# Kernel tuning notes

Measured on AMD Instinct MI355X. Metric: run time of the kernel, lower is better.

The kernel has to match this reference:

```python
import jax, jax.numpy as jnp
import numpy as np

N_USER, N_TX, E = 50000, 50000, 600000
D_USER, D_TX, D_ALIGN, HID, OUT = 128, 64, 128, 256, 128


def setup_inputs() -> dict:
    key = jax.random.key(0)
    ks = jax.random.split(key, 16)
    s = 0.05
    return {
        "x_user": jax.random.normal(ks[0], (N_USER, D_USER), jnp.float32),
        "x_tx": jax.random.normal(ks[1], (N_TX, D_TX), jnp.float32),
        "edge_user_tx": jax.random.randint(ks[2], (2, E), 0, N_USER),
        "edge_tx_user": jax.random.randint(ks[3], (2, E), 0, N_TX),
        "W_align_user": jax.random.normal(ks[4], (D_USER, D_ALIGN), jnp.float32) * s,
        "b_align_user": jnp.zeros((D_ALIGN,), jnp.float32),
        "W_align_tx": jax.random.normal(ks[5], (D_TX, D_ALIGN), jnp.float32) * s,
        "b_align_tx": jnp.zeros((D_ALIGN,), jnp.float32),
        "eps_ut": jnp.zeros((), jnp.float32),
        "eps_tu": jnp.zeros((), jnp.float32),
        "W1_ut": jax.random.normal(ks[6], (D_TX + D_ALIGN, HID), jnp.float32) * s,
        "b1_ut": jnp.zeros((HID,), jnp.float32),
        "W2_ut": jax.random.normal(ks[7], (HID, OUT), jnp.float32) * s,
        "b2_ut": jnp.zeros((OUT,), jnp.float32),
        "W1_tu": jax.random.normal(ks[8], (D_USER + D_ALIGN, HID), jnp.float32) * s,
        "b1_tu": jnp.zeros((HID,), jnp.float32),
        "W2_tu": jax.random.normal(ks[9], (HID, OUT), jnp.float32) * s,
        "b2_tu": jnp.zeros((OUT,), jnp.float32),
    }


def _mlp(h, W1, b1, W2, b2):
    return jnp.maximum(h @ W1 + b1, 0.0) @ W2 + b2


def _hexgin_conv(x_src, x_dst, edge_index, W_a, b_a, eps, W1, b1, W2, b2):
    # align src features, gather along edges, scatter-sum into dst nodes
    a_src = x_src @ W_a + b_a                       # [N_src, D_ALIGN]
    msgs = a_src[edge_index[0]]                     # [E, D_ALIGN] gather
    agg = jax.ops.segment_sum(msgs, edge_index[1], num_segments=x_dst.shape[0])
    h = jnp.concatenate([(1.0 + eps) * x_dst, agg], axis=1)
    return _mlp(h, W1, b1, W2, b2)


def reference(x_user, x_tx, edge_user_tx, edge_tx_user,
              W_align_user, b_align_user, W_align_tx, b_align_tx,
              eps_ut, eps_tu,
              W1_ut, b1_ut, W2_ut, b2_ut,
              W1_tu, b1_tu, W2_tu, b2_tu):
    # relation (user, makes, tx): updates tx nodes
    out_tx = _hexgin_conv(x_user, x_tx, edge_user_tx,
                          W_align_user, b_align_user, eps_ut,
                          W1_ut, b1_ut, W2_ut, b2_ut)
    # relation (tx, to, user): updates user nodes
    out_user = _hexgin_conv(x_tx, x_user, edge_tx_user,
                            W_align_tx, b_align_tx, eps_tu,
                            W1_tu, b1_tu, W2_tu, b2_tu)
    # HeteroConv aggr='sum': single relation per target, so plain outputs
    return out_user, out_tx
```

## Files before the change

kernel.cpp:

```cpp
#include <hip/hip_runtime.h>
#include <hip/hip_bf16.h>


#define D_USER 128
#define D_TX 64
#define D_ALIGN 128
#define HID 256
#define OUT_D 128
#define NNODE 50000
#define SLOTS 64

typedef __attribute__((ext_vector_type(8))) short short8;
typedef __attribute__((ext_vector_type(4))) float f32x4;
typedef unsigned short ush;

struct alignas(8) us4 { ush x, y, z, w; };

__device__ __forceinline__ ush f2bf(float f) {
    union { float f; unsigned u; } v; v.f = f;
    unsigned u = v.u + 0x7fffu + ((v.u >> 16) & 1u);
    return (ush)(u >> 16);
}
__device__ __forceinline__ float2 bfu2f(unsigned u) {
    union { unsigned u; float f; } a, b;
    a.u = (u & 0xffffu) << 16;
    b.u = u & 0xffff0000u;
    return make_float2(a.f, b.f);
}
__device__ __forceinline__ unsigned f2bfu(float2 v) {
    return (unsigned)f2bf(v.x) | ((unsigned)f2bf(v.y) << 16);
}

__global__ void to_bf16_all(const float* __restrict__ xu, ush* __restrict__ xbu,
                            const float* __restrict__ xt, ush* __restrict__ xbt,
                            int n8u, int n8t)
{
    int i = blockIdx.x * blockDim.x + threadIdx.x;
    const float* x; ush* xb; int j;
    if (i < n8u) { x = xu; xb = xbu; j = i; }
    else if (i < n8u + n8t) { x = xt; xb = xbt; j = i - n8u; }
    else return;
    const float4 a = *reinterpret_cast<const float4*>(&x[(size_t)j * 8]);
    const float4 b = *reinterpret_cast<const float4*>(&x[(size_t)j * 8 + 4]);
    ush o[8];
    o[0] = f2bf(a.x); o[1] = f2bf(a.y); o[2] = f2bf(a.z); o[3] = f2bf(a.w);
    o[4] = f2bf(b.x); o[5] = f2bf(b.y); o[6] = f2bf(b.z); o[7] = f2bf(b.w);
    *reinterpret_cast<uint4*>(&xb[(size_t)j * 8]) = *reinterpret_cast<uint4*>(o);
}

__global__ void wprep(const float* __restrict__ Wa_u, const float* __restrict__ ba_u,
                      const float* __restrict__ W1_ut,
                      const float* __restrict__ Wa_t, const float* __restrict__ ba_t,
                      const float* __restrict__ W1_tu,
                      const float* __restrict__ W2_ut, const float* __restrict__ W2_tu,
                      ush* __restrict__ Bt1a, float* __restrict__ bfv1,
                      ush* __restrict__ Bt1b, float* __restrict__ bfv2,
                      ush* __restrict__ Bt2a, ush* __restrict__ Bt2b)
{
    const int KT = 192;
    const int SEG1 = HID * (KT + 1);
    const int SEG2 = OUT_D * HID;
    int idx = blockIdx.x * blockDim.x + threadIdx.x;
    if (idx < 2 * SEG1) {
        bool r2 = idx >= SEG1;
        int id = r2 ? idx - SEG1 : idx;
        const float* Wa = r2 ? Wa_t : Wa_u;
        const float* ba = r2 ? ba_t : ba_u;
        const float* W1 = r2 ? W1_tu : W1_ut;
        ush* Bt = r2 ? Bt1b : Bt1a;
        float* bfv = r2 ? bfv2 : bfv1;
        const int Dd = r2 ? 128 : 64;
        int c = id & (HID - 1);
        int k = id >> 8;
        const float* w1bot = W1 + (size_t)Dd * HID;
        if (k < Dd) {
            Bt[(size_t)c * KT + k] = f2bf(W1[(size_t)k * HID + c]);
        } else if (k < KT) {
            int ks = k - Dd;
            float acc = 0.f;
            for (int j = 0; j < D_ALIGN; ++j)
                acc += Wa[ks * D_ALIGN + j] * w1bot[(size_t)j * HID + c];
            Bt[(size_t)c * KT + k] = f2bf(acc);
        } else {
            float acc = 0.f;
            for (int j = 0; j < D_ALIGN; ++j)
                acc += ba[j] * w1bot[(size_t)j * HID + c];
            bfv[c] = acc;
        }
    } else if (idx < 2 * SEG1 + 2 * SEG2) {
        int id = idx - 2 * SEG1;
        bool r2 = id >= SEG2;
        if (r2) id -= SEG2;
        const float* W2 = r2 ? W2_tu : W2_ut;
        ush* Bt2 = r2 ? Bt2b : Bt2a;
        int c = id & (OUT_D - 1);
        int k = id >> 7;
        Bt2[(size_t)c * HID + k] = f2bf(W2[(size_t)k * OUT_D + c]);
    }
}

__global__ void fill_direct(const int* __restrict__ e_ut, const int* __restrict__ e_tu,
                            int E, int* __restrict__ pad)
{
    int i = blockIdx.x * blockDim.x + threadIdx.x;
    if (i >= 2 * E) return;
    int d, s;
    if (i < E) { d = e_ut[E + i];                    s = e_ut[i]; }
    else       { int j = i - E; d = NNODE + e_tu[E + j]; s = e_tu[j]; }
    int pos = atomicAdd(&pad[(size_t)d * SLOTS], 1);
    if (pos < SLOTS - 1) pad[(size_t)d * SLOTS + 1 + pos] = s;
}

__global__ __launch_bounds__(256) void agg_all(
    const ush* __restrict__ xbu, const ush* __restrict__ xbt,
    const int* __restrict__ pad, ush* __restrict__ Sb1, ush* __restrict__ Sb2)
{
    int w = (blockIdx.x * 256 + threadIdx.x) >> 6;
    if (w >= 2 * NNODE) return;
    const int lane = threadIdx.x & 63;
    const int* slot = pad + (size_t)w * SLOTS;
    const int n = min(slot[0], SLOTS - 1);
    const int idx = (lane < n) ? slot[1 + lane] : 0;
    if (w < NNODE) {
        float2 acc = make_float2(0.f, 0.f);
        int i = 0;
        for (; i + 4 <= n; i += 4) {
            int s0 = __shfl(idx, i),     s1 = __shfl(idx, i + 1);
            int s2 = __shfl(idx, i + 2), s3 = __shfl(idx, i + 3);
            unsigned v0 = *reinterpret_cast<const unsigned*>(&xbu[(size_t)s0 * 128 + 2 * lane]);
            unsigned v1 = *reinterpret_cast<const unsigned*>(&xbu[(size_t)s1 * 128 + 2 * lane]);
            unsigned v2 = *reinterpret_cast<const unsigned*>(&xbu[(size_t)s2 * 128 + 2 * lane]);
            unsigned v3 = *reinterpret_cast<const unsigned*>(&xbu[(size_t)s3 * 128 + 2 * lane]);
            float2 f0 = bfu2f(v0), f1 = bfu2f(v1), f2 = bfu2f(v2), f3 = bfu2f(v3);
            acc.x += (f0.x + f1.x) + (f2.x + f3.x);
            acc.y += (f0.y + f1.y) + (f2.y + f3.y);
        }
        for (; i < n; ++i) {
            int s0 = __shfl(idx, i);
            unsigned v0 = *reinterpret_cast<const unsigned*>(&xbu[(size_t)s0 * 128 + 2 * lane]);
            float2 f0 = bfu2f(v0);
            acc.x += f0.x; acc.y += f0.y;
        }
        *reinterpret_cast<unsigned*>(&Sb1[(size_t)w * 128 + 2 * lane]) = f2bfu(acc);
    } else {
        const int w2 = w - NNODE;
        const int half = lane >> 5, l2 = lane & 31;
        float2 acc = make_float2(0.f, 0.f);
        int i = 0;
        for (; i + 4 <= n; i += 4) {
            int s0 = __shfl(idx, i + half);
            int s1 = __shfl(idx, i + 2 + half);
            unsigned v0 = *reinterpret_cast<const unsigned*>(&xbt[(size_t)s0 * 64 + 2 * l2]);
            unsigned v1 = *reinterpret_cast<const unsigned*>(&xbt[(size_t)s1 * 64 + 2 * l2]);
            float2 f0 = bfu2f(v0), f1 = bfu2f(v1);
            acc.x += f0.x + f1.x;
            acc.y += f0.y + f1.y;
        }
        for (; i + 2 <= n; i += 2) {
            int s0 = __shfl(idx, i + half);
            unsigned v0 = *reinterpret_cast<const unsigned*>(&xbt[(size_t)s0 * 64 + 2 * l2]);
            float2 f0 = bfu2f(v0);
            acc.x += f0.x; acc.y += f0.y;
        }
        if (i < n && half == 0) {
            int s0 = __shfl(idx, i);
            unsigned v0 = *reinterpret_cast<const unsigned*>(&xbt[(size_t)s0 * 64 + 2 * l2]);
            float2 f0 = bfu2f(v0);
            acc.x += f0.x; acc.y += f0.y;
        }
        acc.x += __shfl_xor(acc.x, 32);
        acc.y += __shfl_xor(acc.y, 32);
        if (half == 0)
            *reinterpret_cast<unsigned*>(&Sb2[(size_t)w2 * 64 + 2 * l2]) = f2bfu(acc);
    }
}

__global__ __launch_bounds__(256) void mlp1_all(
    const float* __restrict__ x_tx, const float* __restrict__ x_user,
    const ush* __restrict__ Sb1, const ush* __restrict__ Sb2,
    const ush* __restrict__ Bt1a, const ush* __restrict__ Bt1b,
    const float* __restrict__ bfv1, const float* __restrict__ bfv2,
    const float* __restrict__ b1_ut, const float* __restrict__ b1_tu,
    const int* __restrict__ pad,
    const float* __restrict__ eps_ut, const float* __restrict__ eps_tu,
    ush* __restrict__ hidb1, ush* __restrict__ hidb2, int M, int nb1)
{
    const int KT = 192;
    __shared__ ush As[128 * 40];
    __shared__ ush Bs[128 * 40];
    const int tid = threadIdx.x;
    const bool r2 = (int)blockIdx.y >= nb1;
    const int bm = (r2 ? blockIdx.y - nb1 : blockIdx.y) * 128;
    const int bn = blockIdx.x * 128;
    const float* xdst = r2 ? x_user : x_tx;
    const int Dd = r2 ? 128 : 64;
    const ush* Sb = r2 ? Sb2 : Sb1;
    const int Dsrc = r2 ? 64 : 128;
    const ush* Bt = r2 ? Bt1b : Bt1a;
    const float* bfv = r2 ? bfv2 : bfv1;
    const float* b1 = r2 ? b1_tu : b1_ut;
    const int* dg = pad + (size_t)(r2 ? NNODE : 0) * SLOTS;
    ush* hidb = r2 ? hidb2 : hidb1;
    const float e = 1.f + (r2 ? eps_tu[0] : eps_ut[0]);

    const int lane = tid & 63, wave = tid >> 6;
    const int wm = wave >> 1, wn = wave & 1;
    const int lo = lane & 15, hi = lane >> 4;

    f32x4 acc[4][4];
    #pragma unroll
    for (int m = 0; m < 4; ++m)
        #pragma unroll
        for (int n = 0; n < 4; ++n)
            acc[m][n] = f32x4{0.f, 0.f, 0.f, 0.f};

    for (int k0 = 0; k0 < KT; k0 += 32) {
        if (k0 < Dd) {
            #pragma unroll
            for (int q = 0; q < 4; ++q) {
                int idx = tid + 256 * q;
                int r = idx >> 3, c4 = idx & 7;
                int gr = bm + r;
                float4 v = make_float4(0.f, 0.f, 0.f, 0.f);
                if (gr < M)
                    v = *reinterpret_cast<const float4*>(&xdst[(size_t)gr * Dd + k0 + c4 * 4]);
                us4 u; u.x = f2bf(v.x * e); u.y = f2bf(v.y * e);
                u.z = f2bf(v.z * e); u.w = f2bf(v.w * e);
                *reinterpret_cast<us4*>(&As[r * 40 + c4 * 4]) = u;
            }
        } else {
            int kb = k0 - Dd;
            #pragma unroll
            for (int q = 0; q < 2; ++q) {
                int idx = tid + 256 * q;
                int r = idx >> 2, c8 = idx & 3;
                int gr = bm + r;
                uint4 v = uint4{0u, 0u, 0u, 0u};
                if (gr < M)
                    v = *reinterpret_cast<const uint4*>(&Sb[(size_t)gr * Dsrc + kb + c8 * 8]);
                *reinterpret_cast<uint4*>(&As[r * 40 + c8 * 8]) = v;
            }
        }
        #pragma unroll
        for (int q = 0; q < 2; ++q) {
            int idx = tid + 256 * q;
            int c = idx >> 2, ku = idx & 3;
            uint4 v = *reinterpret_cast<const uint4*>(&Bt[(size_t)(bn + c) * KT + k0 + ku * 8]);
            *reinterpret_cast<uint4*>(&Bs[c * 40 + ku * 8]) = v;
        }
        __syncthreads();
        short8 av[4], bv[4];
        #pragma unroll
        for (int m = 0; m < 4; ++m)
            av[m] = *reinterpret_cast<const short8*>(&As[(wm * 64 + m * 16 + lo) * 40 + hi * 8]);
        #pragma unroll
        for (int n = 0; n < 4; ++n)
            bv[n] = *reinterpret_cast<const short8*>(&Bs[(wn * 64 + n * 16 + lo) * 40 + hi * 8]);
        #pragma unroll
        for (int m = 0; m < 4; ++m)
            #pragma unroll
            for (int n = 0; n < 4; ++n)
                acc[m][n] = __builtin_amdgcn_mfma_f32_16x16x32_bf16(av[m], bv[n], acc[m][n], 0, 0, 0);
        __syncthreads();
    }

    float b1v[4], bfl[4]; int gcv[4];
    #pragma unroll
    for (int n = 0; n < 4; ++n) {
        int gc = bn + wn * 64 + n * 16 + lo;
        gcv[n] = gc; b1v[n] = b1[gc]; bfl[n] = bfv[gc];
    }
    #pragma unroll
    for (int m = 0; m < 4; ++m)
        #pragma unroll
        for (int reg = 0; reg < 4; ++reg) {
            int gr = bm + wm * 64 + m * 16 + hi * 4 + reg;
            if (gr >= M) continue;
            float dgv = (float)dg[(size_t)gr * SLOTS];
            #pragma unroll
            for (int n = 0; n < 4; ++n) {
                float val = acc[m][n][reg] + b1v[n] + dgv * bfl[n];
                hidb[(size_t)gr * HID + gcv[n]] = f2bf(fmaxf(val, 0.f));
            }
        }
}

__global__ __launch_bounds__(256) void mlp2_all(
    const ush* __restrict__ hidb1, const ush* __restrict__ hidb2,
    const ush* __restrict__ Bt2a, const ush* __restrict__ Bt2b,
    const float* __restrict__ b2_ut, const float* __restrict__ b2_tu,
    float* __restrict__ out_tx, float* __restrict__ out_user, int M, int nb1)
{
    const int KT = 256;
    __shared__ ush As[128 * 40];
    __shared__ ush Bs[128 * 40];
    const int tid = threadIdx.x;
    const bool r2 = (int)blockIdx.y >= nb1;
    const int bm = (r2 ? blockIdx.y - nb1 : blockIdx.y) * 128;
    const ush* hidb = r2 ? hidb2 : hidb1;
    const ush* Bt2 = r2 ? Bt2b : Bt2a;
    const float* b2 = r2 ? b2_tu : b2_ut;
    float* out = r2 ? out_user : out_tx;

    const int lane = tid & 63, wave = tid >> 6;
    const int wm = wave >> 1, wn = wave & 1;
    const int lo = lane & 15, hi = lane >> 4;

    f32x4 acc[4][4];
    #pragma unroll
    for (int m = 0; m < 4; ++m)
        #pragma unroll
        for (int n = 0; n < 4; ++n)
            acc[m][n] = f32x4{0.f, 0.f, 0.f, 0.f};

    for (int k0 = 0; k0 < KT; k0 += 32) {
        #pragma unroll
        for (int q = 0; q < 2; ++q) {
            int idx = tid + 256 * q;
            int r = idx >> 2, ku = idx & 3;
            int gr = bm + r;
            uint4 v = uint4{0u, 0u, 0u, 0u};
            if (gr < M)
                v = *reinterpret_cast<const uint4*>(&hidb[(size_t)gr * KT + k0 + ku * 8]);
            *reinterpret_cast<uint4*>(&As[r * 40 + ku * 8]) = v;
        }
        #pragma unroll
        for (int q = 0; q < 2; ++q) {
            int idx = tid + 256 * q;
            int c = idx >> 2, ku = idx & 3;
            uint4 v = *reinterpret_cast<const uint4*>(&Bt2[(size_t)c * KT + k0 + ku * 8]);
            *reinterpret_cast<uint4*>(&Bs[c * 40 + ku * 8]) = v;
        }
        __syncthreads();
        short8 av[4], bv[4];
        #pragma unroll
        for (int m = 0; m < 4; ++m)
            av[m] = *reinterpret_cast<const short8*>(&As[(wm * 64 + m * 16 + lo) * 40 + hi * 8]);
        #pragma unroll
        for (int n = 0; n < 4; ++n)
            bv[n] = *reinterpret_cast<const short8*>(&Bs[(wn * 64 + n * 16 + lo) * 40 + hi * 8]);
        #pragma unroll
        for (int m = 0; m < 4; ++m)
            #pragma unroll
            for (int n = 0; n < 4; ++n)
                acc[m][n] = __builtin_amdgcn_mfma_f32_16x16x32_bf16(av[m], bv[n], acc[m][n], 0, 0, 0);
        __syncthreads();
    }

    float b2v[4]; int gcv[4];
    #pragma unroll
    for (int n = 0; n < 4; ++n) {
        int gc = wn * 64 + n * 16 + lo;
        gcv[n] = gc; b2v[n] = b2[gc];
    }
    #pragma unroll
    for (int m = 0; m < 4; ++m)
        #pragma unroll
        for (int reg = 0; reg < 4; ++reg) {
            int gr = bm + wm * 64 + m * 16 + hi * 4 + reg;
            if (gr >= M) continue;
            #pragma unroll
            for (int n = 0; n < 4; ++n)
                out[(size_t)gr * OUT_D + gcv[n]] = acc[m][n][reg] + b2v[n];
        }
}

extern "C" void kernel_launch(void* const* d_in, const int* in_sizes, int n_in,
                              void* d_out, int out_size, void* d_ws, size_t ws_size,
                              hipStream_t stream)
{
    const float* x_user   = (const float*)d_in[0];
    const float* x_tx     = (const float*)d_in[1];
    const int*   e_ut     = (const int*)d_in[2];
    const int*   e_tu     = (const int*)d_in[3];
    const float* Wa_user  = (const float*)d_in[4];
    const float* ba_user  = (const float*)d_in[5];
    const float* Wa_tx    = (const float*)d_in[6];
    const float* ba_tx    = (const float*)d_in[7];
    const float* eps_ut   = (const float*)d_in[8];
    const float* eps_tu   = (const float*)d_in[9];
    const float* W1_ut    = (const float*)d_in[10];
    const float* b1_ut    = (const float*)d_in[11];
    const float* W2_ut    = (const float*)d_in[12];
    const float* b2_ut    = (const float*)d_in[13];
    const float* W1_tu    = (const float*)d_in[14];
    const float* b1_tu    = (const float*)d_in[15];
    const float* W2_tu    = (const float*)d_in[16];
    const float* b2_tu    = (const float*)d_in[17];

    const int N_user = in_sizes[0] / D_USER;
    const int N_tx   = in_sizes[1] / D_TX;
    const int E      = in_sizes[2] / 2;
    const int NT     = 2 * NNODE;

    float* out_user = (float*)d_out;
    float* out_tx   = (float*)d_out + (size_t)N_user * OUT_D;

    int*   pad   = (int*)d_ws;
    float* fws   = (float*)d_ws;
    ush*   Bt1a  = (ush*)(fws + 6500000);
    ush*   Bt1b  = (ush*)(fws + 6525000);
    ush*   Bt2a  = (ush*)(fws + 6550000);
    ush*   Bt2b  = (ush*)(fws + 6570000);
    float* bfv1  = fws + 6590000;
    float* bfv2  = fws + 6591000;
    ush*   xbu   = (ush*)(fws + 6600000);
    ush*   xbt   = (ush*)(fws + 9800000);
    ush*   Sb1   = (ush*)(fws + 11400000);
    ush*   Sb2   = (ush*)(fws + 14600000);
    ush*   hidb1 = (ush*)(fws + 16200000);
    ush*   hidb2 = (ush*)(fws + 22600000);

    const int threads = 256;
    const int n8u = N_user * D_USER / 8, n8t = N_tx * D_TX / 8;
    const int nb1 = (NNODE + 127) / 128;

    hipMemsetAsync(pad, 0, (size_t)NT * SLOTS * sizeof(int), stream);
    to_bf16_all<<<(n8u + n8t + 255) / 256, threads, 0, stream>>>(
        x_user, xbu, x_tx, xbt, n8u, n8t);
    wprep<<<(2 * HID * 193 + 2 * OUT_D * HID + 255) / 256, threads, 0, stream>>>(
        Wa_user, ba_user, W1_ut, Wa_tx, ba_tx, W1_tu, W2_ut, W2_tu,
        Bt1a, bfv1, Bt1b, bfv2, Bt2a, Bt2b);
    fill_direct<<<(2 * E + 255) / 256, threads, 0, stream>>>(e_ut, e_tu, E, pad);
    agg_all<<<(NT * 64 + 255) / 256, threads, 0, stream>>>(xbu, xbt, pad, Sb1, Sb2);
    dim3 g1(2, 2 * nb1);
    mlp1_all<<<g1, threads, 0, stream>>>(
        x_tx, x_user, Sb1, Sb2, Bt1a, Bt1b, bfv1, bfv2, b1_ut, b1_tu,
        pad, eps_ut, eps_tu, hidb1, hidb2, NNODE, nb1);
    dim3 g2(1, 2 * nb1);
    mlp2_all<<<g2, threads, 0, stream>>>(
        hidb1, hidb2, Bt2a, Bt2b, b2_ut, b2_tu, out_tx, out_user, NNODE, nb1);
}
```

Before: 217.8 us.

## Pack edge slots as 16-bit indices and pipeline relations across fused heterogeneous kernels

Edge source indices are now stored as 16-bit values in a 32-int per-node bucket instead of 64 ints, which halves the adjacency buffer, its memset and the slot reads. The kernel sequence is restructured so each launch mixes independent work from the two relations: fill for one relation runs beside aggregation for the other, aggregation beside the first MLP, and so on, in five launches. This aims to cut launch count and fill idle tail time. The 16-bit indices depend on node counts staying below 65536.

```diff
diff --git a/kernel.cpp b/kernel.cpp
--- a/kernel.cpp
+++ b/kernel.cpp
@@ -8,7 +8,8 @@
 #define HID 256
 #define OUT_D 128
 #define NNODE 50000
-#define SLOTS 64
+#define BI 32
+#define MAXSLOT 62
 
 typedef __attribute__((ext_vector_type(8))) short short8;
 typedef __attribute__((ext_vector_type(4))) float f32x4;
@@ -31,11 +32,21 @@
     return (unsigned)f2bf(v.x) | ((unsigned)f2bf(v.y) << 16);
 }
 
-__global__ void to_bf16_all(const float* __restrict__ xu, ush* __restrict__ xbu,
-                            const float* __restrict__ xt, ush* __restrict__ xbt,
-                            int n8u, int n8t)
-{
-    int i = blockIdx.x * blockDim.x + threadIdx.x;
+
+__device__ __forceinline__ void dev_fill(const int* __restrict__ e, int E, int i,
+                                         int* __restrict__ pad, int dbase)
+{
+    int d = dbase + e[E + i];
+    int s = e[i];
+    int pos = atomicAdd(&pad[(size_t)d * BI], 1);
+    if (pos < MAXSLOT)
+        ((ush*)pad)[(size_t)d * (2 * BI) + 2 + pos] = (ush)s;
+}
+
+__device__ __forceinline__ void dev_to_bf16(int i,
+    const float* __restrict__ xu, ush* __restrict__ xbu,
+    const float* __restrict__ xt, ush* __restrict__ xbt, int n8u, int n8t)
+{
     const float* x; ush* xb; int j;
     if (i < n8u) { x = xu; xb = xbu; j = i; }
     else if (i < n8u + n8t) { x = xt; xb = xbt; j = i - n8u; }
@@ -48,19 +59,19 @@
     *reinterpret_cast<uint4*>(&xb[(size_t)j * 8]) = *reinterpret_cast<uint4*>(o);
 }
 
-__global__ void wprep(const float* __restrict__ Wa_u, const float* __restrict__ ba_u,
-                      const float* __restrict__ W1_ut,
-                      const float* __restrict__ Wa_t, const float* __restrict__ ba_t,
-                      const float* __restrict__ W1_tu,
-                      const float* __restrict__ W2_ut, const float* __restrict__ W2_tu,
-                      ush* __restrict__ Bt1a, float* __restrict__ bfv1,
-                      ush* __restrict__ Bt1b, float* __restrict__ bfv2,
-                      ush* __restrict__ Bt2a, ush* __restrict__ Bt2b)
+__device__ __forceinline__ void dev_wprep(int idx,
+    const float* __restrict__ Wa_u, const float* __restrict__ ba_u,
+    const float* __restrict__ W1_ut,
+    const float* __restrict__ Wa_t, const float* __restrict__ ba_t,
+    const float* __restrict__ W1_tu,
+    const float* __restrict__ W2_ut, const float* __restrict__ W2_tu,
+    ush* __restrict__ Bt1a, float* __restrict__ bfv1,
+    ush* __restrict__ Bt1b, float* __restrict__ bfv2,
+    ush* __restrict__ Bt2a, ush* __restrict__ Bt2b)
 {
     const int KT = 192;
     const int SEG1 = HID * (KT + 1);
     const int SEG2 = OUT_D * HID;
-    int idx = blockIdx.x * blockDim.x + threadIdx.x;
     if (idx < 2 * SEG1) {
         bool r2 = idx >= SEG1;
         int id = r2 ? idx - SEG1 : idx;
@@ -99,113 +110,101 @@
     }
 }
 
-__global__ void fill_direct(const int* __restrict__ e_ut, const int* __restrict__ e_tu,
-                            int E, int* __restrict__ pad)
-{
-    int i = blockIdx.x * blockDim.x + threadIdx.x;
-    if (i >= 2 * E) return;
-    int d, s;
-    if (i < E) { d = e_ut[E + i];                    s = e_ut[i]; }
-    else       { int j = i - E; d = NNODE + e_tu[E + j]; s = e_tu[j]; }
-    int pos = atomicAdd(&pad[(size_t)d * SLOTS], 1);
-    if (pos < SLOTS - 1) pad[(size_t)d * SLOTS + 1 + pos] = s;
-}
-
-__global__ __launch_bounds__(256) void agg_all(
-    const ush* __restrict__ xbu, const ush* __restrict__ xbt,
-    const int* __restrict__ pad, ush* __restrict__ Sb1, ush* __restrict__ Sb2)
-{
-    int w = (blockIdx.x * 256 + threadIdx.x) >> 6;
-    if (w >= 2 * NNODE) return;
-    const int lane = threadIdx.x & 63;
-    const int* slot = pad + (size_t)w * SLOTS;
-    const int n = min(slot[0], SLOTS - 1);
-    const int idx = (lane < n) ? slot[1 + lane] : 0;
-    if (w < NNODE) {
-        float2 acc = make_float2(0.f, 0.f);
-        int i = 0;
-        for (; i + 4 <= n; i += 4) {
-            int s0 = __shfl(idx, i),     s1 = __shfl(idx, i + 1);
-            int s2 = __shfl(idx, i + 2), s3 = __shfl(idx, i + 3);
-            unsigned v0 = *reinterpret_cast<const unsigned*>(&xbu[(size_t)s0 * 128 + 2 * lane]);
-            unsigned v1 = *reinterpret_cast<const unsigned*>(&xbu[(size_t)s1 * 128 + 2 * lane]);
-            unsigned v2 = *reinterpret_cast<const unsigned*>(&xbu[(size_t)s2 * 128 + 2 * lane]);
-            unsigned v3 = *reinterpret_cast<const unsigned*>(&xbu[(size_t)s3 * 128 + 2 * lane]);
-            float2 f0 = bfu2f(v0), f1 = bfu2f(v1), f2 = bfu2f(v2), f3 = bfu2f(v3);
-            acc.x += (f0.x + f1.x) + (f2.x + f3.x);
-            acc.y += (f0.y + f1.y) + (f2.y + f3.y);
-        }
-        for (; i < n; ++i) {
-            int s0 = __shfl(idx, i);
-            unsigned v0 = *reinterpret_cast<const unsigned*>(&xbu[(size_t)s0 * 128 + 2 * lane]);
-            float2 f0 = bfu2f(v0);
-            acc.x += f0.x; acc.y += f0.y;
-        }
-        *reinterpret_cast<unsigned*>(&Sb1[(size_t)w * 128 + 2 * lane]) = f2bfu(acc);
-    } else {
-        const int w2 = w - NNODE;
-        const int half = lane >> 5, l2 = lane & 31;
-        float2 acc = make_float2(0.f, 0.f);
-        int i = 0;
-        for (; i + 4 <= n; i += 4) {
-            int s0 = __shfl(idx, i + half);
-            int s1 = __shfl(idx, i + 2 + half);
-            unsigned v0 = *reinterpret_cast<const unsigned*>(&xbt[(size_t)s0 * 64 + 2 * l2]);
-            unsigned v1 = *reinterpret_cast<const unsigned*>(&xbt[(size_t)s1 * 64 + 2 * l2]);
-            float2 f0 = bfu2f(v0), f1 = bfu2f(v1);
-            acc.x += f0.x + f1.x;
-            acc.y += f0.y + f1.y;
-        }
-        for (; i + 2 <= n; i += 2) {
-            int s0 = __shfl(idx, i + half);
-            unsigned v0 = *reinterpret_cast<const unsigned*>(&xbt[(size_t)s0 * 64 + 2 * l2]);
-            float2 f0 = bfu2f(v0);
-            acc.x += f0.x; acc.y += f0.y;
-        }
-        if (i < n && half == 0) {
-            int s0 = __shfl(idx, i);
-            unsigned v0 = *reinterpret_cast<const unsigned*>(&xbt[(size_t)s0 * 64 + 2 * l2]);
-            float2 f0 = bfu2f(v0);
-            acc.x += f0.x; acc.y += f0.y;
-        }
-        acc.x += __shfl_xor(acc.x, 32);
-        acc.y += __shfl_xor(acc.y, 32);
-        if (half == 0)
-            *reinterpret_cast<unsigned*>(&Sb2[(size_t)w2 * 64 + 2 * l2]) = f2bfu(acc);
-    }
-}
-
-__global__ __launch_bounds__(256) void mlp1_all(
-    const float* __restrict__ x_tx, const float* __restrict__ x_user,
-    const ush* __restrict__ Sb1, const ush* __restrict__ Sb2,
-    const ush* __restrict__ Bt1a, const ush* __restrict__ Bt1b,
-    const float* __restrict__ bfv1, const float* __restrict__ bfv2,
-    const float* __restrict__ b1_ut, const float* __restrict__ b1_tu,
-    const int* __restrict__ pad,
-    const float* __restrict__ eps_ut, const float* __restrict__ eps_tu,
-    ush* __restrict__ hidb1, ush* __restrict__ hidb2, int M, int nb1)
+__device__ __forceinline__ int slot_word(const int* blk, int lane)
+{
+    return ((lane & 31) < 31) ? blk[1 + (lane & 31)] : 0;
+}
+__device__ __forceinline__ int slot_get(int word, int j)
+{
+    return (j & 1) ? ((word >> 16) & 0xffff) : (word & 0xffff);
+}
+
+__device__ __forceinline__ void dev_agg128(int w, int lane,
+    const ush* __restrict__ xbu, const int* __restrict__ pad, ush* __restrict__ Sb1)
+{
+    const int* blk = pad + (size_t)w * BI;
+    const int n = min(blk[0], MAXSLOT);
+    const int word = slot_word(blk, lane);
+    float2 acc = make_float2(0.f, 0.f);
+    int i = 0;
+    for (; i + 4 <= n; i += 4) {
+        int wa = __shfl(word, i >> 1);
+        int wb = __shfl(word, (i >> 1) + 1);
+        int s0 = wa & 0xffff, s1 = (wa >> 16) & 0xffff;
+        int s2 = wb & 0xffff, s3 = (wb >> 16) & 0xffff;
+        unsigned v0 = *reinterpret_cast<const unsigned*>(&xbu[(size_t)s0 * 128 + 2 * lane]);
+        unsigned v1 = *reinterpret_cast<const unsigned*>(&xbu[(size_t)s1 * 128 + 2 * lane]);
+        unsigned v2 = *reinterpret_cast<const unsigned*>(&xbu[(size_t)s2 * 128 + 2 * lane]);
+        unsigned v3 = *reinterpret_cast<const unsigned*>(&xbu[(size_t)s3 * 128 + 2 * lane]);
+        float2 f0 = bfu2f(v0), f1 = bfu2f(v1), f2 = bfu2f(v2), f3 = bfu2f(v3);
+        acc.x += (f0.x + f1.x) + (f2.x + f3.x);
+        acc.y += (f0.y + f1.y) + (f2.y + f3.y);
+    }
+    for (; i < n; ++i) {
+        int ww = __shfl(word, i >> 1);
+        int s0 = slot_get(ww, i);
+        unsigned v0 = *reinterpret_cast<const unsigned*>(&xbu[(size_t)s0 * 128 + 2 * lane]);
+        float2 f0 = bfu2f(v0);
+        acc.x += f0.x; acc.y += f0.y;
+    }
+    *reinterpret_cast<unsigned*>(&Sb1[(size_t)w * 128 + 2 * lane]) = f2bfu(acc);
+}
+
+__device__ __forceinline__ void dev_agg64(int w2, int lane,
+    const ush* __restrict__ xbt, const int* __restrict__ pad, ush* __restrict__ Sb2)
+{
+    const int* blk = pad + (size_t)(NNODE + w2) * BI;
+    const int n = min(blk[0], MAXSLOT);
+    const int word = slot_word(blk, lane);
+    const int half = lane >> 5, l2 = lane & 31;
+    float2 acc = make_float2(0.f, 0.f);
+    int i = 0;
+    for (; i + 4 <= n; i += 4) {
+        int ja = i + half, jb = i + 2 + half;
+        int wa = __shfl(word, ja >> 1);
+        int wb = __shfl(word, jb >> 1);
+        int s0 = slot_get(wa, ja), s1 = slot_get(wb, jb);
+        unsigned v0 = *reinterpret_cast<const unsigned*>(&xbt[(size_t)s0 * 64 + 2 * l2]);
+        unsigned v1 = *reinterpret_cast<const unsigned*>(&xbt[(size_t)s1 * 64 + 2 * l2]);
+        float2 f0 = bfu2f(v0), f1 = bfu2f(v1);
+        acc.x += f0.x + f1.x;
+        acc.y += f0.y + f1.y;
+    }
+    for (; i + 2 <= n; i += 2) {
+        int j = i + half;
+        int ww = __shfl(word, j >> 1);
+        int s0 = slot_get(ww, j);
+        unsigned v0 = *reinterpret_cast<const unsigned*>(&xbt[(size_t)s0 * 64 + 2 * l2]);
+        float2 f0 = bfu2f(v0);
+        acc.x += f0.x; acc.y += f0.y;
+    }
+    if (i < n && half == 0) {
+        int ww = __shfl(word, i >> 1);
+        int s0 = slot_get(ww, i);
+        unsigned v0 = *reinterpret_cast<const unsigned*>(&xbt[(size_t)s0 * 64 + 2 * l2]);
+        float2 f0 = bfu2f(v0);
+        acc.x += f0.x; acc.y += f0.y;
+    }
+    acc.x += __shfl_xor(acc.x, 32);
+    acc.y += __shfl_xor(acc.y, 32);
+    if (half == 0)
+        *reinterpret_cast<unsigned*>(&Sb2[(size_t)w2 * 64 + 2 * l2]) = f2bfu(acc);
+}
+
+__device__ void dev_mlp1(ush* As, ush* Bs, int tid, int bx, int bm,
+    const float* __restrict__ xdst, int Dd,
+    const ush* __restrict__ Sb, int Dsrc,
+    const ush* __restrict__ Bt, const float* __restrict__ bfv,
+    const float* __restrict__ b1, const int* __restrict__ pad, int dbase,
+    const float* __restrict__ eps, ush* __restrict__ hidb)
 {
     const int KT = 192;
-    __shared__ ush As[128 * 40];
-    __shared__ ush Bs[128 * 40];
-    const int tid = threadIdx.x;
-    const bool r2 = (int)blockIdx.y >= nb1;
-    const int bm = (r2 ? blockIdx.y - nb1 : blockIdx.y) * 128;
-    const int bn = blockIdx.x * 128;
-    const float* xdst = r2 ? x_user : x_tx;
-    const int Dd = r2 ? 128 : 64;
-    const ush* Sb = r2 ? Sb2 : Sb1;
-    const int Dsrc = r2 ? 64 : 128;
-    const ush* Bt = r2 ? Bt1b : Bt1a;
-    const float* bfv = r2 ? bfv2 : bfv1;
-    const float* b1 = r2 ? b1_tu : b1_ut;
-    const int* dg = pad + (size_t)(r2 ? NNODE : 0) * SLOTS;
-    ush* hidb = r2 ? hidb2 : hidb1;
-    const float e = 1.f + (r2 ? eps_tu[0] : eps_ut[0]);
-
+    const int M = NNODE;
+    const int bn = bx * 128;
     const int lane = tid & 63, wave = tid >> 6;
     const int wm = wave >> 1, wn = wave & 1;
     const int lo = lane & 15, hi = lane >> 4;
+    const float e = 1.f + eps[0];
 
     f32x4 acc[4][4];
     #pragma unroll
@@ -276,7 +275,7 @@
         for (int reg = 0; reg < 4; ++reg) {
             int gr = bm + wm * 64 + m * 16 + hi * 4 + reg;
             if (gr >= M) continue;
-            float dgv = (float)dg[(size_t)gr * SLOTS];
+            float dgv = (float)pad[(size_t)(dbase + gr) * BI];
             #pragma unroll
             for (int n = 0; n < 4; ++n) {
                 float val = acc[m][n][reg] + b1v[n] + dgv * bfl[n];
@@ -285,23 +284,12 @@
         }
 }
 
-__global__ __launch_bounds__(256) void mlp2_all(
-    const ush* __restrict__ hidb1, const ush* __restrict__ hidb2,
-    const ush* __restrict__ Bt2a, const ush* __restrict__ Bt2b,
-    const float* __restrict__ b2_ut, const float* __restrict__ b2_tu,
-    float* __restrict__ out_tx, float* __restrict__ out_user, int M, int nb1)
+__device__ void dev_mlp2(ush* As, ush* Bs, int tid, int bm,
+    const ush* __restrict__ hidb, const ush* __restrict__ Bt2,
+    const float* __restrict__ b2, float* __restrict__ out)
 {
     const int KT = 256;
-    __shared__ ush As[128 * 40];
-    __shared__ ush Bs[128 * 40];
-    const int tid = threadIdx.x;
-    const bool r2 = (int)blockIdx.y >= nb1;
-    const int bm = (r2 ? blockIdx.y - nb1 : blockIdx.y) * 128;
-    const ush* hidb = r2 ? hidb2 : hidb1;
-    const ush* Bt2 = r2 ? Bt2b : Bt2a;
-    const float* b2 = r2 ? b2_tu : b2_ut;
-    float* out = r2 ? out_user : out_tx;
-
+    const int M = NNODE;
     const int lane = tid & 63, wave = tid >> 6;
     const int wm = wave >> 1, wn = wave & 1;
     const int lo = lane & 15, hi = lane >> 4;
@@ -364,6 +352,96 @@
                 out[(size_t)gr * OUT_D + gcv[n]] = acc[m][n][reg] + b2v[n];
         }
 }
+
+
+__global__ __launch_bounds__(256) void k1(
+    const int* __restrict__ e_ut, int E, int* __restrict__ pad,
+    const float* __restrict__ xu, ush* __restrict__ xbu,
+    const float* __restrict__ xt, ush* __restrict__ xbt, int n8u, int n8t,
+    const float* __restrict__ Wa_u, const float* __restrict__ ba_u,
+    const float* __restrict__ W1_ut,
+    const float* __restrict__ Wa_t, const float* __restrict__ ba_t,
+    const float* __restrict__ W1_tu,
+    const float* __restrict__ W2_ut, const float* __restrict__ W2_tu,
+    ush* __restrict__ Bt1a, float* __restrict__ bfv1,
+    ush* __restrict__ Bt1b, float* __restrict__ bfv2,
+    ush* __restrict__ Bt2a, ush* __restrict__ Bt2b, int gf, int gb)
+{
+    int b = blockIdx.x, tid = threadIdx.x;
+    if (b < gf) {
+        int i = b * 256 + tid;
+        if (i < E) dev_fill(e_ut, E, i, pad, 0);
+    } else if (b < gf + gb) {
+        dev_to_bf16((b - gf) * 256 + tid, xu, xbu, xt, xbt, n8u, n8t);
+    } else {
+        dev_wprep((b - gf - gb) * 256 + tid, Wa_u, ba_u, W1_ut, Wa_t, ba_t,
+                  W1_tu, W2_ut, W2_tu, Bt1a, bfv1, Bt1b, bfv2, Bt2a, Bt2b);
+    }
+}
+
+__global__ __launch_bounds__(256) void k2(
+    const int* __restrict__ e_tu, int E, int* __restrict__ pad,
+    const ush* __restrict__ xbu, ush* __restrict__ Sb1, int gf)
+{
+    int b = blockIdx.x, tid = threadIdx.x;
+    if (b < gf) {
+        int i = b * 256 + tid;
+        if (i < E) dev_fill(e_tu, E, i, pad, NNODE);
+    } else {
+        int w = (b - gf) * 4 + (tid >> 6);
+        if (w < NNODE) dev_agg128(w, tid & 63, xbu, pad, Sb1);
+    }
+}
+
+__global__ __launch_bounds__(256) void k3(
+    const ush* __restrict__ xbt, const int* __restrict__ pad, ush* __restrict__ Sb2,
+    const float* __restrict__ x_tx, const ush* __restrict__ Sb1,
+    const ush* __restrict__ Bt1a, const float* __restrict__ bfv1,
+    const float* __restrict__ b1_ut, const float* __restrict__ eps_ut,
+    ush* __restrict__ hidb1, int ga)
+{
+    __shared__ ush As[128 * 40];
+    __shared__ ush Bs[128 * 40];
+    int b = blockIdx.x, tid = threadIdx.x;
+    if (b < ga) {
+        int w2 = b * 4 + (tid >> 6);
+        if (w2 < NNODE) dev_agg64(w2, tid & 63, xbt, pad, Sb2);
+    } else {
+        int bb = b - ga;
+        dev_mlp1(As, Bs, tid, bb & 1, (bb >> 1) * 128,
+                 x_tx, D_TX, Sb1, D_USER, Bt1a, bfv1, b1_ut, pad, 0, eps_ut, hidb1);
+    }
+}
+
+__global__ __launch_bounds__(256) void k4(
+    const float* __restrict__ x_user, const ush* __restrict__ Sb2,
+    const ush* __restrict__ Bt1b, const float* __restrict__ bfv2,
+    const float* __restrict__ b1_tu, const int* __restrict__ pad,
+    const float* __restrict__ eps_tu, ush* __restrict__ hidb2,
+    const ush* __restrict__ hidb1, const ush* __restrict__ Bt2a,
+    const float* __restrict__ b2_ut, float* __restrict__ out_tx, int gm1)
+{
+    __shared__ ush As[128 * 40];
+    __shared__ ush Bs[128 * 40];
+    int b = blockIdx.x, tid = threadIdx.x;
+    if (b < gm1) {
+        dev_mlp1(As, Bs, tid, b & 1, (b >> 1) * 128,
+                 x_user, D_USER, Sb2, D_TX, Bt1b, bfv2, b1_tu, pad, NNODE,
+                 eps_tu, hidb2);
+    } else {
+        dev_mlp2(As, Bs, tid, (b - gm1) * 128, hidb1, Bt2a, b2_ut, out_tx);
+    }
+}
+
+__global__ __launch_bounds__(256) void k5(
+    const ush* __restrict__ hidb2, const ush* __restrict__ Bt2b,
+    const float* __restrict__ b2_tu, float* __restrict__ out_user)
+{
+    __shared__ ush As[128 * 40];
+    __shared__ ush Bs[128 * 40];
+    dev_mlp2(As, Bs, threadIdx.x, blockIdx.x * 128, hidb2, Bt2b, b2_tu, out_user);
+}
+
 
 extern "C" void kernel_launch(void* const* d_in, const int* in_sizes, int n_in,
                               void* d_out, int out_size, void* d_ws, size_t ws_size,
@@ -398,36 +476,43 @@
 
     int*   pad   = (int*)d_ws;
     float* fws   = (float*)d_ws;
-    ush*   Bt1a  = (ush*)(fws + 6500000);
-    ush*   Bt1b  = (ush*)(fws + 6525000);
-    ush*   Bt2a  = (ush*)(fws + 6550000);
-    ush*   Bt2b  = (ush*)(fws + 6570000);
-    float* bfv1  = fws + 6590000;
-    float* bfv2  = fws + 6591000;
-    ush*   xbu   = (ush*)(fws + 6600000);
-    ush*   xbt   = (ush*)(fws + 9800000);
-    ush*   Sb1   = (ush*)(fws + 11400000);
-    ush*   Sb2   = (ush*)(fws + 14600000);
-    ush*   hidb1 = (ush*)(fws + 16200000);
-    ush*   hidb2 = (ush*)(fws + 22600000);
+    ush*   Bt1a  = (ush*)(fws + 3300000);
+    ush*   Bt1b  = (ush*)(fws + 3330000);
+    ush*   Bt2a  = (ush*)(fws + 3360000);
+    ush*   Bt2b  = (ush*)(fws + 3380000);
+    float* bfv1  = fws + 3400000;
+    float* bfv2  = fws + 3401000;
+    ush*   xbu   = (ush*)(fws + 3410000);
+    ush*   xbt   = (ush*)(fws + 6700000);
+    ush*   Sb1   = (ush*)(fws + 8400000);
+    ush*   Sb2   = (ush*)(fws + 11700000);
+    ush*   hidb1 = (ush*)(fws + 13400000);
+    ush*   hidb2 = (ush*)(fws + 19900000);
 
     const int threads = 256;
     const int n8u = N_user * D_USER / 8, n8t = N_tx * D_TX / 8;
-    const int nb1 = (NNODE + 127) / 128;
-
-    hipMemsetAsync(pad, 0, (size_t)NT * SLOTS * sizeof(int), stream);
-    to_bf16_all<<<(n8u + n8t + 255) / 256, threads, 0, stream>>>(
-        x_user, xbu, x_tx, xbt, n8u, n8t);
-    wprep<<<(2 * HID * 193 + 2 * OUT_D * HID + 255) / 256, threads, 0, stream>>>(
+    const int gf  = (E + 255) / 256;
+    const int gb  = (n8u + n8t + 255) / 256;
+    const int gw  = (2 * HID * 193 + 2 * OUT_D * HID + 255) / 256;
+    const int ga  = (NNODE + 3) / 4;
+    const int gm1 = 2 * ((NNODE + 127) / 128);
+    const int gm2 = (NNODE + 127) / 128;
+
+    hipMemsetAsync(pad, 0, (size_t)NT * BI * sizeof(int), stream);
+
+    k1<<<gf + gb + gw, threads, 0, stream>>>(
+        e_ut, E, pad, x_user, xbu, x_tx, xbt, n8u, n8t,
         Wa_user, ba_user, W1_ut, Wa_tx, ba_tx, W1_tu, W2_ut, W2_tu,
-        Bt1a, bfv1, Bt1b, bfv2, Bt2a, Bt2b);
-    fill_direct<<<(2 * E + 255) / 256, threads, 0, stream>>>(e_ut, e_tu, E, pad);
-    agg_all<<<(NT * 64 + 255) / 256, threads, 0, stream>>>(xbu, xbt, pad, Sb1, Sb2);
-    dim3 g1(2, 2 * nb1);
-    mlp1_all<<<g1, threads, 0, stream>>>(
-        x_tx, x_user, Sb1, Sb2, Bt1a, Bt1b, bfv1, bfv2, b1_ut, b1_tu,
-        pad, eps_ut, eps_tu, hidb1, hidb2, NNODE, nb1);
-    dim3 g2(1, 2 * nb1);
-    mlp2_all<<<g2, threads, 0, stream>>>(
-        hidb1, hidb2, Bt2a, Bt2b, b2_ut, b2_tu, out_tx, out_user, NNODE, nb1);
-}
+        Bt1a, bfv1, Bt1b, bfv2, Bt2a, Bt2b, gf, gb);
+
+    k2<<<gf + ga, threads, 0, stream>>>(e_tu, E, pad, xbu, Sb1, gf);
+
+    k3<<<ga + gm1, threads, 0, stream>>>(
+        xbt, pad, Sb2, x_tx, Sb1, Bt1a, bfv1, b1_ut, eps_ut, hidb1, ga);
+
+    k4<<<gm1 + gm2, threads, 0, stream>>>(
+        x_user, Sb2, Bt1b, bfv2, b1_tu, pad, eps_tu, hidb2,
+        hidb1, Bt2a, b2_ut, out_tx, gm1);
+
+    k5<<<gm2, threads, 0, stream>>>(hidb2, Bt2b, b2_tu, out_user);
+}
```

New measurement: 370.0 us. 1.7x slower.
